# Performance work log

Measured on AMD Instinct MI355X. Metric: run time of the kernel, lower is better.

Reference implementation:

```python
import jax, jax.numpy as jnp
import numpy as np

B, T, C, H = 8, 1024, 768, 12
HD = C // H
EPS = 1e-5
NEG = jnp.finfo(jnp.float32).min


def layer_norm(x, scale, bias):
    mu = jnp.mean(x, axis=-1, keepdims=True)
    var = jnp.mean(jnp.square(x - mu), axis=-1, keepdims=True)
    return (x - mu) * jax.lax.rsqrt(var + EPS) * scale + bias


def setup_inputs() -> dict:
    key = jax.random.key(0)
    ks = jax.random.split(key, 8)
    s = lambda fan_in: 1.0 / np.sqrt(fan_in)
    x = jax.random.normal(ks[0], (B, T, C), dtype=jnp.float32)
    mask = jnp.tril(jnp.ones((T, T), dtype=bool))[None, None, :, :]
    return {
        "x": x,
        "mask": mask,
        "ln1_scale": jnp.ones((C,), jnp.float32),
        "ln1_bias": jnp.zeros((C,), jnp.float32),
        "w_qkv": jax.random.normal(ks[1], (C, 3 * C), jnp.float32) * s(C),
        "b_qkv": jnp.zeros((3 * C,), jnp.float32),
        "w_attn_proj": jax.random.normal(ks[2], (C, C), jnp.float32) * s(C),
        "b_attn_proj": jnp.zeros((C,), jnp.float32),
        "ln2_scale": jnp.ones((C,), jnp.float32),
        "ln2_bias": jnp.zeros((C,), jnp.float32),
        "w_fc": jax.random.normal(ks[3], (C, 4 * C), jnp.float32) * s(C),
        "b_fc": jnp.zeros((4 * C,), jnp.float32),
        "w_mlp_proj": jax.random.normal(ks[4], (4 * C, C), jnp.float32) * s(4 * C),
        "b_mlp_proj": jnp.zeros((C,), jnp.float32),
    }


def reference(x, mask, ln1_scale, ln1_bias, w_qkv, b_qkv, w_attn_proj,
              b_attn_proj, ln2_scale, ln2_bias, w_fc, b_fc, w_mlp_proj,
              b_mlp_proj):
    # --- attention branch (pre-LN) ---
    h = layer_norm(x, ln1_scale, ln1_bias)
    qkv = jnp.einsum('btc,cd->btd', h, w_qkv) + b_qkv      # [B,T,3C]
    qkv = qkv.reshape(B, T, 3 * H, HD)
    q, k, v = jnp.array_split(qkv, 3, axis=2)              # each [B,T,H,HD]
    scale = 1.0 / jnp.sqrt(jnp.float32(HD))
    attn = jnp.einsum('bqhd,bkhd->bhqk', q, k) * scale     # [B,H,T,T]
    attn = jnp.where(mask, attn, NEG)
    attn = jax.nn.softmax(attn, axis=-1)
    ctx = jnp.einsum('bhqk,bkhd->bqhd', attn, v).reshape(B, T, C)
    attn_out = jnp.einsum('btc,cd->btd', ctx, w_attn_proj) + b_attn_proj
    x = x + attn_out
    # --- MLP branch (pre-LN) ---
    h = layer_norm(x, ln2_scale, ln2_bias)
    h = jax.nn.gelu(jnp.einsum('btc,cf->btf', h, w_fc) + b_fc)  # tanh approx, as flax default
    mlp_out = jnp.einsum('btf,fc->btc', h, w_mlp_proj) + b_mlp_proj
    return x + mlp_out
```

## Files before the change

### kernel.cpp

```cpp
#include <hip/hip_runtime.h>
#include <hip/hip_bf16.h>
#include <cstdint>
#include <math.h>

#define BB 8
#define TT 1024
#define CC 768
#define HH 12
#define MROWS (BB*TT)

typedef __hip_bfloat16 bf16;
typedef __attribute__((ext_vector_type(8))) __bf16 bf16x8;
typedef __attribute__((ext_vector_type(4))) float f32x4;

#define MFMA16(a,b,c) __builtin_amdgcn_mfma_f32_16x16x32_bf16(a,b,c,0,0,0)

__device__ __forceinline__ void gload_lds16(const bf16* g, bf16* l) {
  __builtin_amdgcn_global_load_lds(
      (__attribute__((address_space(1))) void*)(g),
      (__attribute__((address_space(3))) void*)(l), 16, 0, 0);
}

__global__ __launch_bounds__(256) void ln_kernel(
    const float* __restrict__ x, const float* __restrict__ scale,
    const float* __restrict__ bias, bf16* __restrict__ out)
{
  int row = blockIdx.x;
  const float* xr = x + (size_t)row * CC;
  float v[3];
  float s = 0.f, s2 = 0.f;
  for (int i = 0; i < 3; i++) {
    v[i] = xr[threadIdx.x + i*256];
    s += v[i]; s2 += v[i]*v[i];
  }
  for (int m = 1; m < 64; m <<= 1) { s += __shfl_xor(s, m); s2 += __shfl_xor(s2, m); }
  __shared__ float ssum[4], ssum2[4];
  int w = threadIdx.x >> 6;
  if ((threadIdx.x & 63) == 0) { ssum[w] = s; ssum2[w] = s2; }
  __syncthreads();
  s = ssum[0]+ssum[1]+ssum[2]+ssum[3];
  s2 = ssum2[0]+ssum2[1]+ssum2[2]+ssum2[3];
  float mu = s * (1.f/CC);
  float var = s2 * (1.f/CC) - mu*mu;
  float rs = rsqrtf(var + 1e-5f);
  bf16* orow = out + (size_t)row * CC;
  for (int i = 0; i < 3; i++) {
    int c = threadIdx.x + i*256;
    orow[c] = __float2bfloat16((v[i]-mu)*rs*scale[c] + bias[c]);
  }
}

__global__ __launch_bounds__(256) void wtrans_kernel(
    const float* __restrict__ src, bf16* __restrict__ dst, int K, int N)
{
  __shared__ float tile[32][33];
  int n0 = blockIdx.x * 32, k0 = blockIdx.y * 32;
  int tx = threadIdx.x & 31, ty = threadIdx.x >> 5;
  for (int i = 0; i < 4; i++)
    tile[ty + i*8][tx] = src[(size_t)(k0 + ty + i*8)*N + n0 + tx];
  __syncthreads();
  for (int i = 0; i < 4; i++)
    dst[(size_t)(n0 + ty + i*8)*K + k0 + tx] = __float2bfloat16(tile[tx][ty + i*8]);
}

__global__ __launch_bounds__(256) void vtrans_kernel(
    const bf16* __restrict__ src, bf16* __restrict__ dst)
{
  __shared__ bf16 tile[64][65];
  int bh = blockIdx.x >> 4, t0 = (blockIdx.x & 15) * 64;
  const bf16* s = src + ((size_t)bh * TT + t0) * 64;
  for (int i = 0; i < 16; i++) {
    int idx = threadIdx.x + i*256;
    tile[idx >> 6][idx & 63] = s[idx];
  }
  __syncthreads();
  bf16* o = dst + (size_t)bh * 64 * TT + t0;
  for (int i = 0; i < 16; i++) {
    int idx = threadIdx.x + i*256;
    int d = idx >> 6, t = idx & 63;
    o[(size_t)d * TT + t] = tile[t][d];
  }
}

template<int EPI>
__global__ __launch_bounds__(256) void gemm_bt(
    const bf16* __restrict__ A, const bf16* __restrict__ Bt,
    const float* __restrict__ bias, int Mdim, int Ndim, int Kdim,
    const float* __restrict__ res, void* __restrict__ out0,
    bf16* __restrict__ outK, bf16* __restrict__ outV)
{
  __shared__ bf16 As[128*32];
  __shared__ bf16 Bs[128*32];
  int tid = threadIdx.x;
  int wave = tid >> 6, lane = tid & 63;
  int quad = lane >> 4, l15 = lane & 15;
  int wr = wave >> 1, wc = wave & 1;
  int m0 = blockIdx.y * 128, n0 = blockIdx.x * 128;
  const int sub = lane >> 2;
  const int kk = (lane & 3) * 8;

  f32x4 acc[4][4];
  for (int i = 0; i < 4; i++) for (int j = 0; j < 4; j++)
    acc[i][j] = (f32x4){0.f,0.f,0.f,0.f};

  for (int kt = 0; kt < Kdim; kt += 32) {
    __syncthreads();
    for (int q = 0; q < 2; q++) {
      int seg = q*4 + wave;
      const bf16* ga = A + (size_t)(m0 + seg*16 + sub) * Kdim + kt + kk;
      gload_lds16(ga, As + seg*512 + lane*8);
      const bf16* gb = Bt + (size_t)(n0 + seg*16 + sub) * Kdim + kt + kk;
      gload_lds16(gb, Bs + seg*512 + lane*8);
    }
    __syncthreads();
    bf16x8 af[4], bfr[4];
    for (int i = 0; i < 4; i++)
      af[i] = *reinterpret_cast<const bf16x8*>(As + (wr*64 + i*16 + l15)*32 + quad*8);
    for (int j = 0; j < 4; j++)
      bfr[j] = *reinterpret_cast<const bf16x8*>(Bs + (wc*64 + j*16 + l15)*32 + quad*8);
    for (int i = 0; i < 4; i++)
      for (int j = 0; j < 4; j++)
        acc[i][j] = MFMA16(af[i], bfr[j], acc[i][j]);
  }

  for (int i = 0; i < 4; i++) {
    for (int j = 0; j < 4; j++) {
      for (int r = 0; r < 4; r++) {
        int row = m0 + wr*64 + i*16 + quad*4 + r;
        int col = n0 + wc*64 + j*16 + l15;
        float cv = acc[i][j][r] + bias[col];
        if (EPI == 0) {
          int part = col / 768;
          int cc = col - part*768;
          int h = cc >> 6, d = cc & 63;
          int b = row >> 10, t = row & 1023;
          bf16* dst = (part == 0) ? (bf16*)out0 : (part == 1) ? outK : outV;
          dst[(((size_t)(b*HH + h))*TT + t)*64 + d] = __float2bfloat16(cv);
        } else if (EPI == 1) {
          ((float*)out0)[(size_t)row*Ndim + col] = cv + res[(size_t)row*Ndim + col];
        } else {
          float u = cv;
          float y = 0.7978845608f*(u + 0.044715f*u*u*u);
          float e = __expf(2.f*fabsf(y));
          float z = 2.f/(e + 1.f);
          float sel = (y >= 0.f) ? (2.f - z) : z;
          ((bf16*)out0)[(size_t)row*Ndim + col] = __float2bfloat16(0.5f*u*sel);
        }
      }
    }
  }
}

__global__ __launch_bounds__(256) void attn_kernel(
    const bf16* __restrict__ Q, const bf16* __restrict__ Kb,
    const bf16* __restrict__ Vt, bf16* __restrict__ ctx)
{
  __shared__ bf16 Ks[64*64];
  __shared__ bf16 Vs[64*64];
  __shared__ bf16 Ps[4*16*64];

  int tid = threadIdx.x, wave = tid >> 6, lane = tid & 63;
  int quad = lane >> 4, l15 = lane & 15;
  int bh = blockIdx.x >> 4;
  int tile = 15 - (blockIdx.x & 15);
  int q0b = tile*64;
  int q0w = q0b + wave*16;
  int b = bh / HH, h = bh - b*HH;
  const bf16* Qp = Q + ((size_t)bh*TT + q0w)*64;
  const bf16* Kp = Kb + (size_t)bh*TT*64;
  const bf16* Vp = Vt + (size_t)bh*64*TT;
  bf16* Pw = Ps + wave*16*64;

  bf16x8 qf[2];
  qf[0] = *reinterpret_cast<const bf16x8*>(Qp + l15*64 + quad*8);
  qf[1] = *reinterpret_cast<const bf16x8*>(Qp + l15*64 + 32 + quad*8);

  f32x4 O[4];
  for (int j = 0; j < 4; j++) O[j] = (f32x4){0.f,0.f,0.f,0.f};
  float lsum[4] = {0.f, 0.f, 0.f, 0.f};
  const float c2 = 0.18033688f;

  const int srow0 = wave*16 + (lane >> 3);
  const int sc    = lane & 7;

  int nc = tile + 1;

  bf16x8 kreg[2], vreg[2], kreg2[2], vreg2[2];
  for (int rep = 0; rep < 2; rep++) {
    int row = srow0 + rep*8;
    kreg[rep] = *reinterpret_cast<const bf16x8*>(Kp + (size_t)row*64 + sc*8);
    vreg[rep] = *reinterpret_cast<const bf16x8*>(Vp + (size_t)row*TT + sc*8);
  }

  for (int ci = 0; ci < nc; ci++) {
    int kbase = ci*64;
    __syncthreads();
    for (int rep = 0; rep < 2; rep++) {
      int row = srow0 + rep*8;
      int ph = sc ^ (row & 7);
      *reinterpret_cast<bf16x8*>(Ks + row*64 + ph*8) = kreg[rep];
      *reinterpret_cast<bf16x8*>(Vs + row*64 + ph*8) = vreg[rep];
    }
    if (ci + 1 < nc) {
      int kb2 = kbase + 64;
      for (int rep = 0; rep < 2; rep++) {
        int row = srow0 + rep*8;
        kreg2[rep] = *reinterpret_cast<const bf16x8*>(Kp + (size_t)(kb2 + row)*64 + sc*8);
        vreg2[rep] = *reinterpret_cast<const bf16x8*>(Vp + (size_t)row*TT + kb2 + sc*8);
      }
    }
    __syncthreads();

    f32x4 S[4];
    for (int j = 0; j < 4; j++) S[j] = (f32x4){0.f,0.f,0.f,0.f};
    for (int kh = 0; kh < 2; kh++) {
      for (int j = 0; j < 4; j++) {
        int key = j*16 + l15;
        bf16x8 kf = *reinterpret_cast<const bf16x8*>(
            Ks + key*64 + ((kh*4 + quad) ^ (key & 7))*8);
        S[j] = MFMA16(qf[kh], kf, S[j]);
      }
    }

    float p[4][4];
    if (kbase + 63 > q0w) {
      for (int j = 0; j < 4; j++) {
        int key = kbase + j*16 + l15;
        for (int r = 0; r < 4; r++) {
          int row = q0w + quad*4 + r;
          p[j][r] = (key <= row) ? __builtin_amdgcn_exp2f(S[j][r]*c2) : 0.f;
        }
      }
    } else {
      for (int j = 0; j < 4; j++)
        for (int r = 0; r < 4; r++)
          p[j][r] = __builtin_amdgcn_exp2f(S[j][r]*c2);
    }
    for (int j = 0; j < 4; j++)
      for (int r = 0; r < 4; r++) lsum[r] += p[j][r];

    for (int j = 0; j < 4; j++) {
      int cblk = j*2 + (l15 >> 3);
      int koff = l15 & 7;
      for (int r = 0; r < 4; r++) {
        int q = quad*4 + r;
        Pw[q*64 + (cblk ^ (q & 7))*8 + koff] = __float2bfloat16(p[j][r]);
      }
    }

    for (int kh = 0; kh < 2; kh++) {
      bf16x8 pf = *reinterpret_cast<const bf16x8*>(
          Pw + l15*64 + ((kh*4 + quad) ^ (l15 & 7))*8);
      for (int j = 0; j < 4; j++) {
        int d = j*16 + l15;
        bf16x8 vf = *reinterpret_cast<const bf16x8*>(
            Vs + d*64 + ((kh*4 + quad) ^ (d & 7))*8);
        O[j] = MFMA16(pf, vf, O[j]);
      }
    }

    for (int rep = 0; rep < 2; rep++) { kreg[rep] = kreg2[rep]; vreg[rep] = vreg2[rep]; }
  }

  for (int r = 0; r < 4; r++)
    for (int msk = 1; msk < 16; msk <<= 1)
      lsum[r] += __shfl_xor(lsum[r], msk);

  bf16* cp = ctx + ((size_t)b*TT + q0w)*CC + h*64;
  for (int r = 0; r < 4; r++) {
    float inv = 1.f / lsum[r];
    int row = quad*4 + r;
    for (int j = 0; j < 4; j++)
      cp[(size_t)row*CC + j*16 + l15] = __float2bfloat16(O[j][r]*inv);
  }
}

extern "C" void kernel_launch(void* const* d_in, const int* in_sizes, int n_in,
                              void* d_out, int out_size, void* d_ws, size_t ws_size,
                              hipStream_t stream)
{
  const float* x    = (const float*)d_in[0];
  const float* ln1s = (const float*)d_in[2];
  const float* ln1b = (const float*)d_in[3];
  const float* wqkv = (const float*)d_in[4];
  const float* bqkv = (const float*)d_in[5];
  const float* wap  = (const float*)d_in[6];
  const float* bap  = (const float*)d_in[7];
  const float* ln2s = (const float*)d_in[8];
  const float* ln2b = (const float*)d_in[9];
  const float* wfc  = (const float*)d_in[10];
  const float* bfc  = (const float*)d_in[11];
  const float* wmp  = (const float*)d_in[12];
  const float* bmp  = (const float*)d_in[13];

  char* ws = (char*)d_ws;
  bf16* wqkv_t = (bf16*)ws; ws += (size_t)2304*768*2;
  bf16* wap_t  = (bf16*)ws; ws += (size_t)768*768*2;
  bf16* wfc_t  = (bf16*)ws; ws += (size_t)3072*768*2;
  bf16* wmp_t  = (bf16*)ws; ws += (size_t)768*3072*2;
  bf16* buf1   = (bf16*)ws; ws += (size_t)MROWS*CC*2;
  bf16* Qb     = (bf16*)ws; ws += (size_t)MROWS*CC*2;
  bf16* Kbuf   = (bf16*)ws; ws += (size_t)MROWS*CC*2;
  bf16* Vb     = (bf16*)ws; ws += (size_t)MROWS*CC*2;
  bf16* Vt     = (bf16*)ws; ws += (size_t)MROWS*CC*2;
  bf16* g      = Qb;
  float* r1    = (float*)ws; ws += (size_t)MROWS*CC*4;

  dim3 blk(256);
  wtrans_kernel<<<dim3(2304/32, 768/32), blk, 0, stream>>>(wqkv, wqkv_t, 768, 2304);
  wtrans_kernel<<<dim3(768/32, 768/32), blk, 0, stream>>>(wap, wap_t, 768, 768);
  wtrans_kernel<<<dim3(3072/32, 768/32), blk, 0, stream>>>(wfc, wfc_t, 768, 3072);
  wtrans_kernel<<<dim3(768/32, 3072/32), blk, 0, stream>>>(wmp, wmp_t, 3072, 768);
  ln_kernel<<<MROWS, blk, 0, stream>>>(x, ln1s, ln1b, buf1);
  gemm_bt<0><<<dim3(2304/128, MROWS/128), blk, 0, stream>>>(
      buf1, wqkv_t, bqkv, MROWS, 2304, 768, nullptr, (void*)Qb, Kbuf, Vb);
  vtrans_kernel<<<BB*HH*16, blk, 0, stream>>>(Vb, Vt);
  attn_kernel<<<BB*HH*16, blk, 0, stream>>>(Qb, Kbuf, Vt, buf1);
  gemm_bt<1><<<dim3(768/128, MROWS/128), blk, 0, stream>>>(
      buf1, wap_t, bap, MROWS, 768, 768, x, (void*)r1, nullptr, nullptr);
  ln_kernel<<<MROWS, blk, 0, stream>>>(r1, ln2s, ln2b, buf1);
  gemm_bt<2><<<dim3(3072/128, MROWS/128), blk, 0, stream>>>(
      buf1, wfc_t, bfc, MROWS, 3072, 768, nullptr, (void*)g, nullptr, nullptr);
  gemm_bt<1><<<dim3(768/128, MROWS/128), blk, 0, stream>>>(
      g, wmp_t, bmp, MROWS, 768, 3072, r1, d_out, nullptr, nullptr);
}
```

Before: 420.8 us.

## Double-buffer LDS tiles in bf16 GEMM and swizzle block order for L2 reuse

```diff
diff --git a/kernel.cpp b/kernel.cpp
--- a/kernel.cpp
+++ b/kernel.cpp
@@ -89,13 +89,20 @@
     const float* __restrict__ res, void* __restrict__ out0,
     bf16* __restrict__ outK, bf16* __restrict__ outV)
 {
-  __shared__ bf16 As[128*32];
-  __shared__ bf16 Bs[128*32];
+  __shared__ bf16 As[2][128*32];
+  __shared__ bf16 Bs[2][128*32];
   int tid = threadIdx.x;
   int wave = tid >> 6, lane = tid & 63;
   int quad = lane >> 4, l15 = lane & 15;
   int wr = wave >> 1, wc = wave & 1;
-  int m0 = blockIdx.y * 128, n0 = blockIdx.x * 128;
+
+  int Nb = gridDim.x;
+  int lin = blockIdx.y * Nb + blockIdx.x;
+  int band = lin / (8*Nb);
+  int rem  = lin - band*8*Nb;
+  int m0 = (band*8 + (rem & 7)) * 128;
+  int n0 = (rem >> 3) * 128;
+
   const int sub = lane >> 2;
   const int kk = (lane & 3) * 8;
 
@@ -103,21 +110,31 @@
   for (int i = 0; i < 4; i++) for (int j = 0; j < 4; j++)
     acc[i][j] = (f32x4){0.f,0.f,0.f,0.f};
 
-  for (int kt = 0; kt < Kdim; kt += 32) {
+  const int niter = Kdim >> 5;
+  for (int q = 0; q < 2; q++) {
+    int seg = q*4 + wave;
+    gload_lds16(A + (size_t)(m0 + seg*16 + sub) * Kdim + kk, As[0] + seg*512 + lane*8);
+    gload_lds16(Bt + (size_t)(n0 + seg*16 + sub) * Kdim + kk, Bs[0] + seg*512 + lane*8);
+  }
+
+  for (int it = 0; it < niter; it++) {
+    int cur = it & 1, nxt = cur ^ 1;
     __syncthreads();
-    for (int q = 0; q < 2; q++) {
-      int seg = q*4 + wave;
-      const bf16* ga = A + (size_t)(m0 + seg*16 + sub) * Kdim + kt + kk;
-      gload_lds16(ga, As + seg*512 + lane*8);
-      const bf16* gb = Bt + (size_t)(n0 + seg*16 + sub) * Kdim + kt + kk;
-      gload_lds16(gb, Bs + seg*512 + lane*8);
-    }
-    __syncthreads();
+    if (it + 1 < niter) {
+      int kt = (it + 1) << 5;
+      for (int q = 0; q < 2; q++) {
+        int seg = q*4 + wave;
+        gload_lds16(A + (size_t)(m0 + seg*16 + sub) * Kdim + kt + kk,
+                    As[nxt] + seg*512 + lane*8);
+        gload_lds16(Bt + (size_t)(n0 + seg*16 + sub) * Kdim + kt + kk,
+                    Bs[nxt] + seg*512 + lane*8);
+      }
+    }
     bf16x8 af[4], bfr[4];
     for (int i = 0; i < 4; i++)
-      af[i] = *reinterpret_cast<const bf16x8*>(As + (wr*64 + i*16 + l15)*32 + quad*8);
+      af[i] = *reinterpret_cast<const bf16x8*>(As[cur] + (wr*64 + i*16 + l15)*32 + quad*8);
     for (int j = 0; j < 4; j++)
-      bfr[j] = *reinterpret_cast<const bf16x8*>(Bs + (wc*64 + j*16 + l15)*32 + quad*8);
+      bfr[j] = *reinterpret_cast<const bf16x8*>(Bs[cur] + (wc*64 + j*16 + l15)*32 + quad*8);
     for (int i = 0; i < 4; i++)
       for (int j = 0; j < 4; j++)
         acc[i][j] = MFMA16(af[i], bfr[j], acc[i][j]);
```

Result: faster. 398.5 us (-5.3%).

## Pre-pack GEMM operands into MFMA fragment layout and load directly to registers

Applied to the files above, without the earlier changes.

```diff
diff --git a/kernel.cpp b/kernel.cpp
--- a/kernel.cpp
+++ b/kernel.cpp
@@ -15,13 +15,13 @@
 
 #define MFMA16(a,b,c) __builtin_amdgcn_mfma_f32_16x16x32_bf16(a,b,c,0,0,0)
 
-__device__ __forceinline__ void gload_lds16(const bf16* g, bf16* l) {
-  __builtin_amdgcn_global_load_lds(
-      (__attribute__((address_space(1))) void*)(g),
-      (__attribute__((address_space(3))) void*)(l), 16, 0, 0);
-}
-
-__global__ __launch_bounds__(256) void ln_kernel(
+__device__ __forceinline__ void packed_store(bf16* __restrict__ P, int m, int k,
+                                             int Kt32, bf16 v) {
+  P[((size_t)(m >> 4) * Kt32 + (k >> 5)) * 512 +
+    ((m & 15) + 16 * ((k >> 3) & 3)) * 8 + (k & 7)] = v;
+}
+
+__global__ __launch_bounds__(256) void ln_pack_kernel(
     const float* __restrict__ x, const float* __restrict__ scale,
     const float* __restrict__ bias, bf16* __restrict__ out)
 {
@@ -43,24 +43,27 @@
   float mu = s * (1.f/CC);
   float var = s2 * (1.f/CC) - mu*mu;
   float rs = rsqrtf(var + 1e-5f);
-  bf16* orow = out + (size_t)row * CC;
   for (int i = 0; i < 3; i++) {
     int c = threadIdx.x + i*256;
-    orow[c] = __float2bfloat16((v[i]-mu)*rs*scale[c] + bias[c]);
-  }
-}
-
-__global__ __launch_bounds__(256) void wtrans_kernel(
+    packed_store(out, row, c, CC/32,
+                 __float2bfloat16((v[i]-mu)*rs*scale[c] + bias[c]));
+  }
+}
+
+__global__ __launch_bounds__(256) void wpack_kernel(
     const float* __restrict__ src, bf16* __restrict__ dst, int K, int N)
 {
-  __shared__ float tile[32][33];
-  int n0 = blockIdx.x * 32, k0 = blockIdx.y * 32;
-  int tx = threadIdx.x & 31, ty = threadIdx.x >> 5;
-  for (int i = 0; i < 4; i++)
-    tile[ty + i*8][tx] = src[(size_t)(k0 + ty + i*8)*N + n0 + tx];
-  __syncthreads();
-  for (int i = 0; i < 4; i++)
-    dst[(size_t)(n0 + ty + i*8)*K + k0 + tx] = __float2bfloat16(tile[tx][ty + i*8]);
+  int lane = threadIdx.x & 63;
+  int kt = blockIdx.y*4 + (threadIdx.x >> 6);
+  int nt = blockIdx.x;
+  int Kt = K >> 5;
+  int n = nt*16 + (lane & 15);
+  int k0 = kt*32 + (lane >> 4)*8;
+  bf16 vals[8];
+  for (int e = 0; e < 8; e++)
+    vals[e] = __float2bfloat16(src[(size_t)(k0 + e)*N + n]);
+  *reinterpret_cast<bf16x8*>(dst + ((size_t)nt*Kt + kt)*512 + lane*8) =
+      *reinterpret_cast<bf16x8*>(vals);
 }
 
 __global__ __launch_bounds__(256) void vtrans_kernel(
@@ -83,44 +86,55 @@
 }
 
 template<int EPI>
-__global__ __launch_bounds__(256) void gemm_bt(
-    const bf16* __restrict__ A, const bf16* __restrict__ Bt,
-    const float* __restrict__ bias, int Mdim, int Ndim, int Kdim,
+__global__ __launch_bounds__(256) void gemm_pk(
+    const bf16* __restrict__ A, const bf16* __restrict__ B,
+    const float* __restrict__ bias, int Ndim, int Kdim,
     const float* __restrict__ res, void* __restrict__ out0,
     bf16* __restrict__ outK, bf16* __restrict__ outV)
 {
-  __shared__ bf16 As[128*32];
-  __shared__ bf16 Bs[128*32];
   int tid = threadIdx.x;
   int wave = tid >> 6, lane = tid & 63;
   int quad = lane >> 4, l15 = lane & 15;
   int wr = wave >> 1, wc = wave & 1;
-  int m0 = blockIdx.y * 128, n0 = blockIdx.x * 128;
-  const int sub = lane >> 2;
-  const int kk = (lane & 3) * 8;
+
+  int Nb = gridDim.x;
+  int lin = blockIdx.y * Nb + blockIdx.x;
+  int band = lin / (8*Nb);
+  int rem  = lin - band*8*Nb;
+  int m0 = (band*8 + (rem & 7)) * 128;
+  int n0 = (rem >> 3) * 128;
+
+  const int Kt = Kdim >> 5;
+  const bf16* baseA[4];
+  const bf16* baseB[4];
+  for (int i = 0; i < 4; i++)
+    baseA[i] = A + (size_t)((m0 >> 4) + wr*4 + i) * Kt * 512;
+  for (int j = 0; j < 4; j++)
+    baseB[j] = B + (size_t)((n0 >> 4) + wc*4 + j) * Kt * 512;
 
   f32x4 acc[4][4];
   for (int i = 0; i < 4; i++) for (int j = 0; j < 4; j++)
     acc[i][j] = (f32x4){0.f,0.f,0.f,0.f};
 
-  for (int kt = 0; kt < Kdim; kt += 32) {
-    __syncthreads();
-    for (int q = 0; q < 2; q++) {
-      int seg = q*4 + wave;
-      const bf16* ga = A + (size_t)(m0 + seg*16 + sub) * Kdim + kt + kk;
-      gload_lds16(ga, As + seg*512 + lane*8);
-      const bf16* gb = Bt + (size_t)(n0 + seg*16 + sub) * Kdim + kt + kk;
-      gload_lds16(gb, Bs + seg*512 + lane*8);
-    }
-    __syncthreads();
-    bf16x8 af[4], bfr[4];
-    for (int i = 0; i < 4; i++)
-      af[i] = *reinterpret_cast<const bf16x8*>(As + (wr*64 + i*16 + l15)*32 + quad*8);
-    for (int j = 0; j < 4; j++)
-      bfr[j] = *reinterpret_cast<const bf16x8*>(Bs + (wc*64 + j*16 + l15)*32 + quad*8);
+  size_t voff = (size_t)lane * 8;
+  bf16x8 ca[4], cb[4], na[4], nb[4];
+  for (int i = 0; i < 4; i++) ca[i] = *reinterpret_cast<const bf16x8*>(baseA[i] + voff);
+  for (int j = 0; j < 4; j++) cb[j] = *reinterpret_cast<const bf16x8*>(baseB[j] + voff);
+
+  for (int kt = 0; kt < Kt; kt += 2) {
+    for (int i = 0; i < 4; i++) na[i] = *reinterpret_cast<const bf16x8*>(baseA[i] + voff + 512);
+    for (int j = 0; j < 4; j++) nb[j] = *reinterpret_cast<const bf16x8*>(baseB[j] + voff + 512);
     for (int i = 0; i < 4; i++)
       for (int j = 0; j < 4; j++)
-        acc[i][j] = MFMA16(af[i], bfr[j], acc[i][j]);
+        acc[i][j] = MFMA16(ca[i], cb[j], acc[i][j]);
+    if (kt + 2 < Kt) {
+      for (int i = 0; i < 4; i++) ca[i] = *reinterpret_cast<const bf16x8*>(baseA[i] + voff + 1024);
+      for (int j = 0; j < 4; j++) cb[j] = *reinterpret_cast<const bf16x8*>(baseB[j] + voff + 1024);
+    }
+    for (int i = 0; i < 4; i++)
+      for (int j = 0; j < 4; j++)
+        acc[i][j] = MFMA16(na[i], nb[j], acc[i][j]);
+    voff += 1024;
   }
 
   for (int i = 0; i < 4; i++) {
@@ -144,7 +158,8 @@
           float e = __expf(2.f*fabsf(y));
           float z = 2.f/(e + 1.f);
           float sel = (y >= 0.f) ? (2.f - z) : z;
-          ((bf16*)out0)[(size_t)row*Ndim + col] = __float2bfloat16(0.5f*u*sel);
+          packed_store((bf16*)out0, row, col, Ndim >> 5,
+                       __float2bfloat16(0.5f*u*sel));
         }
       }
     }
@@ -266,12 +281,12 @@
     for (int msk = 1; msk < 16; msk <<= 1)
       lsum[r] += __shfl_xor(lsum[r], msk);
 
-  bf16* cp = ctx + ((size_t)b*TT + q0w)*CC + h*64;
   for (int r = 0; r < 4; r++) {
     float inv = 1.f / lsum[r];
-    int row = quad*4 + r;
+    int m = b*TT + q0w + quad*4 + r;
     for (int j = 0; j < 4; j++)
-      cp[(size_t)row*CC + j*16 + l15] = __float2bfloat16(O[j][r]*inv);
+      packed_store(ctx, m, h*64 + j*16 + l15, CC/32,
+                   __float2bfloat16(O[j][r]*inv));
   }
 }
 
@@ -307,20 +322,20 @@
   float* r1    = (float*)ws; ws += (size_t)MROWS*CC*4;
 
   dim3 blk(256);
-  wtrans_kernel<<<dim3(2304/32, 768/32), blk, 0, stream>>>(wqkv, wqkv_t, 768, 2304);
-  wtrans_kernel<<<dim3(768/32, 768/32), blk, 0, stream>>>(wap, wap_t, 768, 768);
-  wtrans_kernel<<<dim3(3072/32, 768/32), blk, 0, stream>>>(wfc, wfc_t, 768, 3072);
-  wtrans_kernel<<<dim3(768/32, 3072/32), blk, 0, stream>>>(wmp, wmp_t, 3072, 768);
-  ln_kernel<<<MROWS, blk, 0, stream>>>(x, ln1s, ln1b, buf1);
-  gemm_bt<0><<<dim3(2304/128, MROWS/128), blk, 0, stream>>>(
-      buf1, wqkv_t, bqkv, MROWS, 2304, 768, nullptr, (void*)Qb, Kbuf, Vb);
+  wpack_kernel<<<dim3(2304/16, 768/128), blk, 0, stream>>>(wqkv, wqkv_t, 768, 2304);
+  wpack_kernel<<<dim3(768/16, 768/128), blk, 0, stream>>>(wap, wap_t, 768, 768);
+  wpack_kernel<<<dim3(3072/16, 768/128), blk, 0, stream>>>(wfc, wfc_t, 768, 3072);
+  wpack_kernel<<<dim3(768/16, 3072/128), blk, 0, stream>>>(wmp, wmp_t, 3072, 768);
+  ln_pack_kernel<<<MROWS, blk, 0, stream>>>(x, ln1s, ln1b, buf1);
+  gemm_pk<0><<<dim3(2304/128, MROWS/128), blk, 0, stream>>>(
+      buf1, wqkv_t, bqkv, 2304, 768, nullptr, (void*)Qb, Kbuf, Vb);
   vtrans_kernel<<<BB*HH*16, blk, 0, stream>>>(Vb, Vt);
   attn_kernel<<<BB*HH*16, blk, 0, stream>>>(Qb, Kbuf, Vt, buf1);
-  gemm_bt<1><<<dim3(768/128, MROWS/128), blk, 0, stream>>>(
-      buf1, wap_t, bap, MROWS, 768, 768, x, (void*)r1, nullptr, nullptr);
-  ln_kernel<<<MROWS, blk, 0, stream>>>(r1, ln2s, ln2b, buf1);
-  gemm_bt<2><<<dim3(3072/128, MROWS/128), blk, 0, stream>>>(
-      buf1, wfc_t, bfc, MROWS, 3072, 768, nullptr, (void*)g, nullptr, nullptr);
-  gemm_bt<1><<<dim3(768/128, MROWS/128), blk, 0, stream>>>(
-      g, wmp_t, bmp, MROWS, 768, 3072, r1, d_out, nullptr, nullptr);
-}
+  gemm_pk<1><<<dim3(768/128, MROWS/128), blk, 0, stream>>>(
+      buf1, wap_t, bap, 768, 768, x, (void*)r1, nullptr, nullptr);
+  ln_pack_kernel<<<MROWS, blk, 0, stream>>>(r1, ln2s, ln2b, buf1);
+  gemm_pk<2><<<dim3(3072/128, MROWS/128), blk, 0, stream>>>(
+      buf1, wfc_t, bfc, 3072, 768, nullptr, (void*)g, nullptr, nullptr);
+  gemm_pk<1><<<dim3(768/128, MROWS/128), blk, 0, stream>>>(
+      g, wmp_t, bmp, 768, 3072, r1, d_out, nullptr, nullptr);
+}
```

After: 443.6 us. 1.05x slower.
